# Kernel optimization log

Hardware: AMD Instinct MI355X
Metric: run time of the kernel (lower is better)

## Reference

```python
import jax, jax.numpy as jnp
import numpy as np
from math import sqrt

D_MODEL = 1024
N_HEADS = 16
E = D_MODEL // N_HEADS  # d_keys = d_values = 64


def setup_inputs() -> dict:
    key = jax.random.key(0)
    ks = jax.random.split(key, 11)
    B, L, S = 2, 2048, 2048
    s = 1.0 / sqrt(D_MODEL)
    return {
        "queries": jax.random.normal(ks[0], (B, L, D_MODEL), jnp.float32),
        "keys": jax.random.normal(ks[1], (B, S, D_MODEL), jnp.float32),
        "values": jax.random.normal(ks[2], (B, S, D_MODEL), jnp.float32),
        "Wq": jax.random.normal(ks[3], (D_MODEL, D_MODEL), jnp.float32) * s,
        "bq": jnp.zeros((D_MODEL,), jnp.float32),
        "Wk": jax.random.normal(ks[4], (D_MODEL, D_MODEL), jnp.float32) * s,
        "bk": jnp.zeros((D_MODEL,), jnp.float32),
        "Wv": jax.random.normal(ks[5], (D_MODEL, D_MODEL), jnp.float32) * s,
        "bv": jnp.zeros((D_MODEL,), jnp.float32),
        "Wo": jax.random.normal(ks[6], (D_MODEL, D_MODEL), jnp.float32) * s,
        "bo": jnp.zeros((D_MODEL,), jnp.float32),
    }


def reference(queries, keys, values, Wq, bq, Wk, bk, Wv, bv, Wo, bo):
    B, L, _ = queries.shape
    S = keys.shape[1]
    H = N_HEADS
    # projections -> [B, L/S, H, E]
    q = (queries @ Wq + bq).reshape(B, L, H, E)
    k = (keys @ Wk + bk).reshape(B, S, H, E)
    v = (values @ Wv + bv).reshape(B, S, H, E)
    scale = 1.0 / sqrt(E)
    scores = jnp.einsum('blhe,bshe->bhls', q, k)  # [B,H,L,S]
    A = jax.nn.softmax(scale * scores, axis=-1)   # dropout = identity (eval)
    V = jnp.einsum('bhls,bshd->blhd', A, v)       # [B,L,H,E]
    out = V.reshape(B, L, H * E) @ Wo + bo
    return out
```

## Files before the change

kernel.cpp:

```cpp
#include <hip/hip_runtime.h>
#include <hip/hip_bf16.h>
#include <stdint.h>

#define BATCH 2
#define SEQ   2048
#define DM    1024
#define NH    16
#define EH    64
#define MROWS (BATCH*SEQ)

typedef __attribute__((ext_vector_type(8))) short  short8;
typedef __attribute__((ext_vector_type(4))) float  floatx4;
typedef __attribute__((ext_vector_type(8))) unsigned short ushort8v;
typedef __attribute__((ext_vector_type(4))) unsigned short ushort4v;

__device__ __forceinline__ unsigned short f2bf(float f) {
    return (unsigned short)((__float_as_uint(f) + 0x8000u) >> 16);
}

__device__ __forceinline__ void gload_lds16(const void* g, void* l) {
    __builtin_amdgcn_global_load_lds(
        (const __attribute__((address_space(1))) unsigned int*)g,
        (__attribute__((address_space(3))) unsigned int*)l, 16, 0, 0);
}

__global__ __launch_bounds__(256)
void transpose_w(const float* __restrict__ W0, const float* __restrict__ W1,
                 const float* __restrict__ W2, const float* __restrict__ W3,
                 unsigned short* __restrict__ T0, unsigned short* __restrict__ T1,
                 unsigned short* __restrict__ T2, unsigned short* __restrict__ T3,
                 int zbase)
{
    int z = zbase + blockIdx.z;
    const float* W = (z == 0) ? W0 : (z == 1) ? W1 : (z == 2) ? W2 : W3;
    unsigned short* T = (z == 0) ? T0 : (z == 1) ? T1 : (z == 2) ? T2 : T3;
    __shared__ float t[32][33];
    const int tid = threadIdx.x;
    const int k0 = blockIdx.y * 32, n0 = blockIdx.x * 32;
    {
        int r = tid >> 3, c4 = (tid & 7) * 4;
        float4 u = *(const float4*)&W[(size_t)(k0 + r) * DM + n0 + c4];
        t[r][c4 + 0] = u.x; t[r][c4 + 1] = u.y; t[r][c4 + 2] = u.z; t[r][c4 + 3] = u.w;
    }
    __syncthreads();
    {
        int n = tid >> 3, k4 = (tid & 7) * 4;
        ushort4v o;
        o[0] = f2bf(t[k4 + 0][n]); o[1] = f2bf(t[k4 + 1][n]);
        o[2] = f2bf(t[k4 + 2][n]); o[3] = f2bf(t[k4 + 3][n]);
        *(ushort4v*)&T[(size_t)(n0 + n) * DM + k0 + k4] = o;
    }
}

struct ProjArgs {
    const float* act[3];
    const unsigned short* wt[3];
    const float* bias[3];
    unsigned short* C[3];
    float oscale[3];
};

__global__ __launch_bounds__(256)
void proj_qkv(ProjArgs pa)
{
    const int z = blockIdx.z;
    const bool vt = (z == 2);
    const int linear = (int)(blockIdx.x + gridDim.x * blockIdx.y);
    int rb, cb;
    if (!vt) { rb = linear & 31; cb = linear >> 5; }
    else     { cb = linear & 31; rb = linear >> 5; }
    const int row0 = rb * 128, col0 = cb * 128;

    const float* act = pa.act[z];
    const unsigned short* wt = pa.wt[z];
    const int actBase = vt ? col0 : row0;
    const int wtBase  = vt ? row0 : col0;

    __shared__ unsigned short As[2][128 * 32];
    __shared__ unsigned short Bs[2][128 * 32];
    unsigned short* conv[2] = { vt ? Bs[0] : As[0], vt ? Bs[1] : As[1] };
    unsigned short* wdst[2] = { vt ? As[0] : Bs[0], vt ? As[1] : Bs[1] };

    const int tid = threadIdx.x;
    const int lane = tid & 63, w = tid >> 6;
    const int lane15 = lane & 15, quad = lane >> 4;
    const int wr = (w >> 1) * 64, wc = (w & 1) * 64;

    floatx4 acc[4][4] = {};

    float4 pre[4];
    const int arow = tid >> 2;
    const int acol = (tid & 3) * 8;

    auto loadPre = [&](int kt) {
        const float* p0 = &act[(size_t)(actBase + arow) * DM + kt + acol];
        const float* p1 = &act[(size_t)(actBase + 64 + arow) * DM + kt + acol];
        pre[0] = *(const float4*)p0; pre[1] = *(const float4*)(p0 + 4);
        pre[2] = *(const float4*)p1; pre[3] = *(const float4*)(p1 + 4);
    };
    auto cvtStore = [&](unsigned short* dst) {
#pragma unroll
        for (int rr = 0; rr < 2; ++rr) {
            int row = rr * 64 + arow;
            int cp = (tid & 3) ^ ((row >> 1) & 3);
            float4 u0 = pre[rr * 2], u1 = pre[rr * 2 + 1];
            ushort8v o8;
            o8[0] = f2bf(u0.x); o8[1] = f2bf(u0.y); o8[2] = f2bf(u0.z); o8[3] = f2bf(u0.w);
            o8[4] = f2bf(u1.x); o8[5] = f2bf(u1.y); o8[6] = f2bf(u1.z); o8[7] = f2bf(u1.w);
            *(ushort8v*)&dst[(size_t)(row * 4 + cp) * 8] = o8;
        }
    };
    auto stageW = [&](int kt, unsigned short* dst) {
#pragma unroll
        for (int rr = 0; rr < 2; ++rr) {
            int p = rr * 256 + w * 64 + lane;
            int row = p >> 2;
            int gch = (p & 3) ^ ((row >> 1) & 3);
            gload_lds16(&wt[(size_t)(wtBase + row) * DM + kt + gch * 8],
                        (char*)dst + (size_t)(rr * 256 + w * 64) * 16);
        }
    };

    loadPre(0);
    stageW(0, wdst[0]);
    cvtStore(conv[0]);
    loadPre(32);
    __syncthreads();

    const int sw = (lane15 >> 1) & 3;
    for (int kt = 0; kt < DM; kt += 32) {
        const int cur = (kt >> 5) & 1, nxt = cur ^ 1;
        if (kt + 32 < DM) {
            stageW(kt + 32, wdst[nxt]);
            cvtStore(conv[nxt]);
            if (kt + 64 < DM) loadPre(kt + 64);
        }

        const unsigned short* as = As[cur];
        const unsigned short* bs = Bs[cur];
        short8 af[4], bf[4];
#pragma unroll
        for (int i = 0; i < 4; ++i)
            af[i] = *(const short8*)&as[(size_t)(wr + i * 16 + lane15) * 32 + ((quad ^ sw) << 3)];
#pragma unroll
        for (int j = 0; j < 4; ++j)
            bf[j] = *(const short8*)&bs[(size_t)(wc + j * 16 + lane15) * 32 + ((quad ^ sw) << 3)];
#pragma unroll
        for (int i = 0; i < 4; ++i)
#pragma unroll
            for (int j = 0; j < 4; ++j)
                acc[i][j] = __builtin_amdgcn_mfma_f32_16x16x32_bf16(af[i], bf[j], acc[i][j], 0, 0, 0);
        __syncthreads();
    }

    const float* bias = pa.bias[z];
    const float os = pa.oscale[z];
    unsigned short* C = pa.C[z];
#pragma unroll
    for (int i = 0; i < 4; ++i) {
#pragma unroll
        for (int j = 0; j < 4; ++j) {
#pragma unroll
            for (int r = 0; r < 4; ++r) {
                int row = row0 + wr + i * 16 + quad * 4 + r;
                int col = col0 + wc + j * 16 + lane15;
                if (!vt) {
                    float v = (acc[i][j][r] + bias[col]) * os;
                    int b = row >> 11, l = row & (SEQ - 1);
                    int h = col >> 6,  e = col & (EH - 1);
                    C[((size_t)(b * NH + h) * SEQ + l) * EH + e] = f2bf(v);
                } else {
                    float v = acc[i][j][r] + bias[row];
                    int h = row >> 6,  e = row & (EH - 1);
                    int b = col >> 11, l = col & (SEQ - 1);
                    C[((size_t)(b * NH + h) * EH + e) * SEQ + l] = f2bf(v);
                }
            }
        }
    }
}

__global__ __launch_bounds__(256)
void gemm_out(const unsigned short* __restrict__ ctx,
              const unsigned short* __restrict__ WoT,
              const float* __restrict__ bo,
              float* __restrict__ out)
{
    const int linear = (int)(blockIdx.x + gridDim.x * blockIdx.y);
    const int rb = linear & 31, cb = linear >> 5;
    const int row0 = rb * 128, col0 = cb * 64;

    __shared__ unsigned short As[2][128 * 32];
    __shared__ unsigned short Bs[2][64 * 32];

    const int tid = threadIdx.x;
    const int lane = tid & 63, w = tid >> 6;
    const int lane15 = lane & 15, quad = lane >> 4;

    floatx4 acc[2][4] = {};

    auto stageA = [&](int kt, unsigned short* dst) {
#pragma unroll
        for (int rr = 0; rr < 2; ++rr) {
            int p = rr * 256 + w * 64 + lane;
            int row = p >> 2;
            int gch = (p & 3) ^ ((row >> 1) & 3);
            gload_lds16(&ctx[(size_t)(row0 + row) * DM + kt + gch * 8],
                        (char*)dst + (size_t)(rr * 256 + w * 64) * 16);
        }
    };
    auto stageB = [&](int kt, unsigned short* dst) {
        int p = w * 64 + lane;
        int row = p >> 2;
        int gch = (p & 3) ^ ((row >> 1) & 3);
        gload_lds16(&WoT[(size_t)(col0 + row) * DM + kt + gch * 8],
                    (char*)dst + (size_t)(w * 64) * 16);
    };

    stageA(0, As[0]);
    stageB(0, Bs[0]);
    __syncthreads();

    const int sw = (lane15 >> 1) & 3;
    for (int kt = 0; kt < DM; kt += 32) {
        const int cur = (kt >> 5) & 1, nxt = cur ^ 1;
        if (kt + 32 < DM) {
            stageA(kt + 32, As[nxt]);
            stageB(kt + 32, Bs[nxt]);
        }

        const unsigned short* as = As[cur];
        const unsigned short* bs = Bs[cur];
        short8 af[2], bf[4];
#pragma unroll
        for (int i = 0; i < 2; ++i)
            af[i] = *(const short8*)&as[(size_t)(w * 32 + i * 16 + lane15) * 32 + ((quad ^ sw) << 3)];
#pragma unroll
        for (int j = 0; j < 4; ++j)
            bf[j] = *(const short8*)&bs[(size_t)(j * 16 + lane15) * 32 + ((quad ^ sw) << 3)];
#pragma unroll
        for (int i = 0; i < 2; ++i)
#pragma unroll
            for (int j = 0; j < 4; ++j)
                acc[i][j] = __builtin_amdgcn_mfma_f32_16x16x32_bf16(af[i], bf[j], acc[i][j], 0, 0, 0);
        __syncthreads();
    }

#pragma unroll
    for (int i = 0; i < 2; ++i)
#pragma unroll
        for (int j = 0; j < 4; ++j)
#pragma unroll
            for (int r = 0; r < 4; ++r) {
                int row = row0 + w * 32 + i * 16 + quad * 4 + r;
                int col = col0 + j * 16 + lane15;
                out[(size_t)row * DM + col] = acc[i][j][r] + bo[col];
            }
}

__device__ __forceinline__ void stage_kv(const unsigned short* __restrict__ Kp,
                                         const unsigned short* __restrict__ Vp,
                                         int st, unsigned short* ksb, unsigned short* vsb,
                                         int w, int lane)
{
#pragma unroll
    for (int rr = 0; rr < 2; ++rr) {
        int p = rr * 256 + w * 64 + lane;
        int row = p >> 3;
        int gch = (p & 7) ^ (row & 7);
        gload_lds16(&Kp[(size_t)(st + row) * EH + gch * 8],
                    ksb + (size_t)(rr * 256 + w * 64) * 8);
        gload_lds16(&Vp[(size_t)row * SEQ + st + gch * 8],
                    vsb + (size_t)(rr * 256 + w * 64) * 8);
    }
}

__global__ __launch_bounds__(256)
void attn_mfma(const unsigned short* __restrict__ Qh,
               const unsigned short* __restrict__ Kh,
               const unsigned short* __restrict__ Vt,
               unsigned short* __restrict__ ctx)
{
    __shared__ unsigned short Ks[2][64 * 64];
    __shared__ unsigned short Vs[2][64 * 64];
    __shared__ unsigned short Ps[128][72];

    const int tid = threadIdx.x;
    const int lane = tid & 63, w = tid >> 6;
    const int lane15 = lane & 15, quad = lane >> 4;

    const int linear = (int)(blockIdx.x + 16 * (blockIdx.y + 16 * blockIdx.z));
    const int bhid = linear & 31;
    const int qt = linear >> 5;
    const int h = bhid & 15, b = bhid >> 4;

    const size_t bh = (size_t)(b * NH + h);
    const unsigned short* Kp = Kh + bh * SEQ * EH;
    const unsigned short* Vp = Vt + bh * EH * SEQ;

    short8 qf[2][2];
    {
        const unsigned short* Qp =
            Qh + (bh * SEQ + (size_t)qt * 128 + w * 32 + lane15) * EH;
#pragma unroll
        for (int ks = 0; ks < 2; ++ks) {
            qf[0][ks] = *(const short8*)(Qp + ks * 32 + quad * 8);
            qf[1][ks] = *(const short8*)(Qp + 16 * EH + ks * 32 + quad * 8);
        }
    }
    short8 ones;
#pragma unroll
    for (int i = 0; i < 8; ++i) ones[i] = (short)0x3F80;

    floatx4 o[2][4] = {};
    floatx4 lacc[2] = {};

    stage_kv(Kp, Vp, 0, Ks[0], Vs[0], w, lane);
    __syncthreads();
    int cur = 0;

    for (int st = 0; st < SEQ; st += 64) {
        int nxt = cur ^ 1;
        if (st + 64 < SEQ)
            stage_kv(Kp, Vp, st + 64, Ks[nxt], Vs[nxt], w, lane);
        const unsigned short* ksb = Ks[cur];
        const unsigned short* vsb = Vs[cur];

        floatx4 sacc[4][2] = {};
#pragma unroll
        for (int ts = 0; ts < 4; ++ts) {
#pragma unroll
            for (int ks = 0; ks < 2; ++ks) {
                short8 kf = *(const short8*)&ksb[((ts * 16 + lane15) << 6) +
                                                 ((((ks << 2) + quad) ^ (lane15 & 7)) << 3)];
                sacc[ts][0] = __builtin_amdgcn_mfma_f32_16x16x32_bf16(kf, qf[0][ks], sacc[ts][0], 0, 0, 0);
                sacc[ts][1] = __builtin_amdgcn_mfma_f32_16x16x32_bf16(kf, qf[1][ks], sacc[ts][1], 0, 0, 0);
            }
        }

#pragma unroll
        for (int ts = 0; ts < 4; ++ts)
#pragma unroll
            for (int nq = 0; nq < 2; ++nq) {
                unsigned int u0 = __float_as_uint(__builtin_amdgcn_exp2f(sacc[ts][nq][0])) + 0x8000u;
                unsigned int u1 = __float_as_uint(__builtin_amdgcn_exp2f(sacc[ts][nq][1])) + 0x8000u;
                unsigned int u2 = __float_as_uint(__builtin_amdgcn_exp2f(sacc[ts][nq][2])) + 0x8000u;
                unsigned int u3 = __float_as_uint(__builtin_amdgcn_exp2f(sacc[ts][nq][3])) + 0x8000u;
                uint2 pk;
                pk.x = (u0 >> 16) | (u1 & 0xFFFF0000u);
                pk.y = (u2 >> 16) | (u3 & 0xFFFF0000u);
                *(uint2*)&Ps[w * 32 + nq * 16 + lane15][ts * 16 + quad * 4] = pk;
            }

#pragma unroll
        for (int ks = 0; ks < 2; ++ks) {
            short8 pf[2];
#pragma unroll
            for (int mt = 0; mt < 2; ++mt) {
                pf[mt] = *(const short8*)&Ps[w * 32 + mt * 16 + lane15][ks * 32 + quad * 8];
                lacc[mt] = __builtin_amdgcn_mfma_f32_16x16x32_bf16(pf[mt], ones, lacc[mt], 0, 0, 0);
            }
#pragma unroll
            for (int t2 = 0; t2 < 4; ++t2) {
                short8 vf = *(const short8*)&vsb[((t2 * 16 + lane15) << 6) +
                                                 ((((ks << 2) + quad) ^ (lane15 & 7)) << 3)];
                o[0][t2] = __builtin_amdgcn_mfma_f32_16x16x32_bf16(pf[0], vf, o[0][t2], 0, 0, 0);
                o[1][t2] = __builtin_amdgcn_mfma_f32_16x16x32_bf16(pf[1], vf, o[1][t2], 0, 0, 0);
            }
        }
        __syncthreads();
        cur = nxt;
    }

#pragma unroll
    for (int mt = 0; mt < 2; ++mt) {
        float inv[4];
#pragma unroll
        for (int r = 0; r < 4; ++r) inv[r] = 1.0f / lacc[mt][r];
#pragma unroll
        for (int t2 = 0; t2 < 4; ++t2)
#pragma unroll
            for (int r = 0; r < 4; ++r) {
                int q = qt * 128 + w * 32 + mt * 16 + quad * 4 + r;
                int col = h * EH + t2 * 16 + lane15;
                ctx[((size_t)(b * SEQ + q)) * DM + col] = f2bf(o[mt][t2][r] * inv[r]);
            }
    }
}

extern "C" void kernel_launch(void* const* d_in, const int* in_sizes, int n_in,
                              void* d_out, int out_size, void* d_ws, size_t ws_size,
                              hipStream_t stream)
{
    const float* queries = (const float*)d_in[0];
    const float* keys    = (const float*)d_in[1];
    const float* values  = (const float*)d_in[2];
    const float* Wq = (const float*)d_in[3];
    const float* bq = (const float*)d_in[4];
    const float* Wk = (const float*)d_in[5];
    const float* bk = (const float*)d_in[6];
    const float* Wv = (const float*)d_in[7];
    const float* bv = (const float*)d_in[8];
    const float* Wo = (const float*)d_in[9];
    const float* bo = (const float*)d_in[10];
    float* out = (float*)d_out;

    unsigned short* ws = (unsigned short*)d_ws;
    const size_t MAT = (size_t)MROWS * DM;
    const size_t WSZ = (size_t)DM * DM;
    unsigned short* Qhp = ws;
    unsigned short* Khp = ws + MAT;
    unsigned short* Vtp = ws + 2 * MAT;
    unsigned short* ctx = ws + 3 * MAT;
    unsigned short* WqT = ctx;
    unsigned short* WkT = ctx + WSZ;
    unsigned short* WvT = ctx + 2 * WSZ;
    unsigned short* WoT = ws;

    const float qscale = 0.125f * 1.44269504088896f;

    transpose_w<<<dim3(DM / 32, DM / 32, 3), 256, 0, stream>>>(
        Wq, Wk, Wv, Wo, WqT, WkT, WvT, WoT, 0);

    ProjArgs pa;
    pa.act[0] = queries; pa.act[1] = keys; pa.act[2] = values;
    pa.wt[0] = WqT;      pa.wt[1] = WkT;   pa.wt[2] = WvT;
    pa.bias[0] = bq;     pa.bias[1] = bk;  pa.bias[2] = bv;
    pa.C[0] = Qhp;       pa.C[1] = Khp;    pa.C[2] = Vtp;
    pa.oscale[0] = qscale; pa.oscale[1] = 1.f; pa.oscale[2] = 1.f;
    proj_qkv<<<dim3(8, 32, 3), 256, 0, stream>>>(pa);

    attn_mfma<<<dim3(SEQ / 128, NH, BATCH), 256, 0, stream>>>(Qhp, Khp, Vtp, ctx);

    transpose_w<<<dim3(DM / 32, DM / 32, 1), 256, 0, stream>>>(
        Wq, Wk, Wv, Wo, WqT, WkT, WvT, WoT, 3);

    gemm_out<<<dim3(16, 32), 256, 0, stream>>>(ctx, WoT, bo, out);
}
```

Before: 274.3 us.

## Use single-buffered BK=64 tiles with 8-chunk XOR swizzle in projection GEMMs

Both the QKV projection and output projection GEMMs change from double-buffered BK=32 LDS tiles to single-buffered BK=64 tiles. This halves the number of K iterations and barriers per tile and widens the swizzle to eight 16-byte chunks per row. The output GEMM also moves to a 2x2 wave layout (64x32 per wave) so each wave reuses more A/B fragments. The cost is that prefetch of the next weight tile into LDS no longer overlaps compute, since each iteration syncs, stages, and syncs again. Only the fp32 activation register prefetch still overlaps.

```diff
diff --git a/kernel.cpp b/kernel.cpp
--- a/kernel.cpp
+++ b/kernel.cpp
@@ -76,10 +76,10 @@
     const int actBase = vt ? col0 : row0;
     const int wtBase  = vt ? row0 : col0;
 
-    __shared__ unsigned short As[2][128 * 32];
-    __shared__ unsigned short Bs[2][128 * 32];
-    unsigned short* conv[2] = { vt ? Bs[0] : As[0], vt ? Bs[1] : As[1] };
-    unsigned short* wdst[2] = { vt ? As[0] : Bs[0], vt ? As[1] : Bs[1] };
+    __shared__ unsigned short As[128 * 64];
+    __shared__ unsigned short Bs[128 * 64];
+    unsigned short* conv = vt ? Bs : As;
+    unsigned short* wdst = vt ? As : Bs;
 
     const int tid = threadIdx.x;
     const int lane = tid & 63, w = tid >> 6;
@@ -88,69 +88,70 @@
 
     floatx4 acc[4][4] = {};
 
-    float4 pre[4];
-    const int arow = tid >> 2;
-    const int acol = (tid & 3) * 8;
+    const int ar = tid >> 1, kh = tid & 1;
+    float4 pre[8];
 
     auto loadPre = [&](int kt) {
-        const float* p0 = &act[(size_t)(actBase + arow) * DM + kt + acol];
-        const float* p1 = &act[(size_t)(actBase + 64 + arow) * DM + kt + acol];
-        pre[0] = *(const float4*)p0; pre[1] = *(const float4*)(p0 + 4);
-        pre[2] = *(const float4*)p1; pre[3] = *(const float4*)(p1 + 4);
+        const float* p = &act[(size_t)(actBase + ar) * DM + kt + kh * 32];
+#pragma unroll
+        for (int j = 0; j < 8; ++j) pre[j] = ((const float4*)p)[j];
     };
-    auto cvtStore = [&](unsigned short* dst) {
-#pragma unroll
-        for (int rr = 0; rr < 2; ++rr) {
-            int row = rr * 64 + arow;
-            int cp = (tid & 3) ^ ((row >> 1) & 3);
-            float4 u0 = pre[rr * 2], u1 = pre[rr * 2 + 1];
+    auto cvtStore = [&]() {
+#pragma unroll
+        for (int j = 0; j < 4; ++j) {
+            int c = kh * 4 + j;
+            int slot = c ^ (ar & 7);
+            float4 u0 = pre[2 * j], u1 = pre[2 * j + 1];
             ushort8v o8;
             o8[0] = f2bf(u0.x); o8[1] = f2bf(u0.y); o8[2] = f2bf(u0.z); o8[3] = f2bf(u0.w);
             o8[4] = f2bf(u1.x); o8[5] = f2bf(u1.y); o8[6] = f2bf(u1.z); o8[7] = f2bf(u1.w);
-            *(ushort8v*)&dst[(size_t)(row * 4 + cp) * 8] = o8;
+            *(ushort8v*)&conv[(size_t)(ar * 8 + slot) * 8] = o8;
         }
     };
-    auto stageW = [&](int kt, unsigned short* dst) {
-#pragma unroll
-        for (int rr = 0; rr < 2; ++rr) {
+    auto stageW = [&](int kt) {
+#pragma unroll
+        for (int rr = 0; rr < 4; ++rr) {
             int p = rr * 256 + w * 64 + lane;
-            int row = p >> 2;
-            int gch = (p & 3) ^ ((row >> 1) & 3);
+            int row = p >> 3;
+            int gch = (p & 7) ^ (row & 7);
             gload_lds16(&wt[(size_t)(wtBase + row) * DM + kt + gch * 8],
-                        (char*)dst + (size_t)(rr * 256 + w * 64) * 16);
+                        (char*)wdst + (size_t)(rr * 256 + w * 64) * 16);
         }
     };
 
     loadPre(0);
-    stageW(0, wdst[0]);
-    cvtStore(conv[0]);
-    loadPre(32);
-    __syncthreads();
-
-    const int sw = (lane15 >> 1) & 3;
-    for (int kt = 0; kt < DM; kt += 32) {
-        const int cur = (kt >> 5) & 1, nxt = cur ^ 1;
-        if (kt + 32 < DM) {
-            stageW(kt + 32, wdst[nxt]);
-            cvtStore(conv[nxt]);
-            if (kt + 64 < DM) loadPre(kt + 64);
-        }
-
-        const unsigned short* as = As[cur];
-        const unsigned short* bs = Bs[cur];
-        short8 af[4], bf[4];
+    for (int kt = 0; kt < DM; kt += 64) {
+        __syncthreads();
+        stageW(kt);
+        cvtStore();
+        __syncthreads();
+        if (kt + 64 < DM) loadPre(kt + 64);
+
+        short8 af[4][2], bf[4][2];
+#pragma unroll
+        for (int i = 0; i < 4; ++i) {
+            int row = wr + i * 16 + lane15;
+#pragma unroll
+            for (int ks = 0; ks < 2; ++ks)
+                af[i][ks] = *(const short8*)&As[(size_t)(row * 8 +
+                                (((ks << 2) + quad) ^ (lane15 & 7))) * 8];
+        }
+#pragma unroll
+        for (int j = 0; j < 4; ++j) {
+            int row = wc + j * 16 + lane15;
+#pragma unroll
+            for (int ks = 0; ks < 2; ++ks)
+                bf[j][ks] = *(const short8*)&Bs[(size_t)(row * 8 +
+                                (((ks << 2) + quad) ^ (lane15 & 7))) * 8];
+        }
 #pragma unroll
         for (int i = 0; i < 4; ++i)
-            af[i] = *(const short8*)&as[(size_t)(wr + i * 16 + lane15) * 32 + ((quad ^ sw) << 3)];
-#pragma unroll
-        for (int j = 0; j < 4; ++j)
-            bf[j] = *(const short8*)&bs[(size_t)(wc + j * 16 + lane15) * 32 + ((quad ^ sw) << 3)];
-#pragma unroll
-        for (int i = 0; i < 4; ++i)
 #pragma unroll
             for (int j = 0; j < 4; ++j)
-                acc[i][j] = __builtin_amdgcn_mfma_f32_16x16x32_bf16(af[i], bf[j], acc[i][j], 0, 0, 0);
-        __syncthreads();
+#pragma unroll
+                for (int ks = 0; ks < 2; ++ks)
+                    acc[i][j] = __builtin_amdgcn_mfma_f32_16x16x32_bf16(
+                        af[i][ks], bf[j][ks], acc[i][j], 0, 0, 0);
     }
 
     const float* bias = pa.bias[z];
@@ -190,70 +191,76 @@
     const int rb = linear & 31, cb = linear >> 5;
     const int row0 = rb * 128, col0 = cb * 64;
 
-    __shared__ unsigned short As[2][128 * 32];
-    __shared__ unsigned short Bs[2][64 * 32];
+    __shared__ unsigned short As[128 * 64];
+    __shared__ unsigned short Bs[64 * 64];
 
     const int tid = threadIdx.x;
     const int lane = tid & 63, w = tid >> 6;
     const int lane15 = lane & 15, quad = lane >> 4;
-
-    floatx4 acc[2][4] = {};
-
-    auto stageA = [&](int kt, unsigned short* dst) {
+    const int wr = (w >> 1) * 64, wc = (w & 1) * 32;
+
+    floatx4 acc[4][2] = {};
+
+    auto stageA = [&](int kt) {
+#pragma unroll
+        for (int rr = 0; rr < 4; ++rr) {
+            int p = rr * 256 + w * 64 + lane;
+            int row = p >> 3, gch = (p & 7) ^ (row & 7);
+            gload_lds16(&ctx[(size_t)(row0 + row) * DM + kt + gch * 8],
+                        (char*)As + (size_t)(rr * 256 + w * 64) * 16);
+        }
+    };
+    auto stageB = [&](int kt) {
 #pragma unroll
         for (int rr = 0; rr < 2; ++rr) {
             int p = rr * 256 + w * 64 + lane;
-            int row = p >> 2;
-            int gch = (p & 3) ^ ((row >> 1) & 3);
-            gload_lds16(&ctx[(size_t)(row0 + row) * DM + kt + gch * 8],
-                        (char*)dst + (size_t)(rr * 256 + w * 64) * 16);
+            int row = p >> 3, gch = (p & 7) ^ (row & 7);
+            gload_lds16(&WoT[(size_t)(col0 + row) * DM + kt + gch * 8],
+                        (char*)Bs + (size_t)(rr * 256 + w * 64) * 16);
         }
     };
-    auto stageB = [&](int kt, unsigned short* dst) {
-        int p = w * 64 + lane;
-        int row = p >> 2;
-        int gch = (p & 3) ^ ((row >> 1) & 3);
-        gload_lds16(&WoT[(size_t)(col0 + row) * DM + kt + gch * 8],
-                    (char*)dst + (size_t)(w * 64) * 16);
-    };
-
-    stageA(0, As[0]);
-    stageB(0, Bs[0]);
-    __syncthreads();
-
-    const int sw = (lane15 >> 1) & 3;
-    for (int kt = 0; kt < DM; kt += 32) {
-        const int cur = (kt >> 5) & 1, nxt = cur ^ 1;
-        if (kt + 32 < DM) {
-            stageA(kt + 32, As[nxt]);
-            stageB(kt + 32, Bs[nxt]);
-        }
-
-        const unsigned short* as = As[cur];
-        const unsigned short* bs = Bs[cur];
-        short8 af[2], bf[4];
-#pragma unroll
-        for (int i = 0; i < 2; ++i)
-            af[i] = *(const short8*)&as[(size_t)(w * 32 + i * 16 + lane15) * 32 + ((quad ^ sw) << 3)];
-#pragma unroll
-        for (int j = 0; j < 4; ++j)
-            bf[j] = *(const short8*)&bs[(size_t)(j * 16 + lane15) * 32 + ((quad ^ sw) << 3)];
-#pragma unroll
-        for (int i = 0; i < 2; ++i)
-#pragma unroll
-            for (int j = 0; j < 4; ++j)
-                acc[i][j] = __builtin_amdgcn_mfma_f32_16x16x32_bf16(af[i], bf[j], acc[i][j], 0, 0, 0);
+
+    for (int kt = 0; kt < DM; kt += 64) {
         __syncthreads();
-    }
-
-#pragma unroll
-    for (int i = 0; i < 2; ++i)
-#pragma unroll
-        for (int j = 0; j < 4; ++j)
+        stageA(kt);
+        stageB(kt);
+        __syncthreads();
+
+        short8 af[4][2], bf[2][2];
+#pragma unroll
+        for (int i = 0; i < 4; ++i) {
+            int row = wr + i * 16 + lane15;
+#pragma unroll
+            for (int ks = 0; ks < 2; ++ks)
+                af[i][ks] = *(const short8*)&As[(size_t)(row * 8 +
+                                (((ks << 2) + quad) ^ (lane15 & 7))) * 8];
+        }
+#pragma unroll
+        for (int j = 0; j < 2; ++j) {
+            int row = wc + j * 16 + lane15;
+#pragma unroll
+            for (int ks = 0; ks < 2; ++ks)
+                bf[j][ks] = *(const short8*)&Bs[(size_t)(row * 8 +
+                                (((ks << 2) + quad) ^ (lane15 & 7))) * 8];
+        }
+#pragma unroll
+        for (int i = 0; i < 4; ++i)
+#pragma unroll
+            for (int j = 0; j < 2; ++j)
+#pragma unroll
+                for (int ks = 0; ks < 2; ++ks)
+                    acc[i][j] = __builtin_amdgcn_mfma_f32_16x16x32_bf16(
+                        af[i][ks], bf[j][ks], acc[i][j], 0, 0, 0);
+    }
+
+#pragma unroll
+    for (int i = 0; i < 4; ++i)
+#pragma unroll
+        for (int j = 0; j < 2; ++j)
 #pragma unroll
             for (int r = 0; r < 4; ++r) {
-                int row = row0 + w * 32 + i * 16 + quad * 4 + r;
-                int col = col0 + j * 16 + lane15;
+                int row = row0 + wr + i * 16 + quad * 4 + r;
+                int col = col0 + wc + j * 16 + lane15;
                 out[(size_t)row * DM + col] = acc[i][j][r] + bo[col];
             }
 }
```

Result: faster. 268.0 us (-2.3%).
